# Kernel tuning notes

Hardware: AMD Instinct MI355X
Metric: run time of the kernel (lower is better)

Reference implementation:

```python
import jax, jax.numpy as jnp
import numpy as np

N_NODES = 100000
N_EDGES = 1600000
IN_DIM = 8
EMB = 50
NUM_TASK = 112
NUM_LAYER = 2
BN_EPS = 1e-5


def setup_inputs() -> dict:
    key = jax.random.key(0)
    ks = jax.random.split(key, 12)
    s = 0.1  # weight init scale
    L, D = NUM_LAYER, EMB
    return {
        "src": jax.random.randint(ks[0], (N_EDGES,), 0, N_NODES),
        "dst": jax.random.randint(ks[1], (N_EDGES,), 0, N_NODES),
        "node_feats": jax.random.normal(ks[2], (N_NODES, IN_DIM), jnp.float32),
        "edge_feats": jax.random.normal(ks[3], (N_EDGES, IN_DIM), jnp.float32),
        "node_W": jax.random.normal(ks[4], (IN_DIM, D), jnp.float32) * s,
        "node_b": jnp.zeros((D,), jnp.float32),
        "edge_W": jax.random.normal(ks[5], (IN_DIM, D), jnp.float32) * s,
        "edge_b": jnp.zeros((D,), jnp.float32),
        "eps": jnp.zeros((L,), jnp.float32),
        "W1": jax.random.normal(ks[6], (L, D, 2 * D), jnp.float32) * s,
        "b1": jnp.zeros((L, 2 * D), jnp.float32),
        "g1": jnp.ones((L, 2 * D), jnp.float32),
        "be1": jnp.zeros((L, 2 * D), jnp.float32),
        "W2": jax.random.normal(ks[7], (L, 2 * D, D), jnp.float32) * s,
        "b2": jnp.zeros((L, D), jnp.float32),
        "g2": jnp.ones((L, D), jnp.float32),
        "be2": jnp.zeros((L, D), jnp.float32),
        "pred_W": jax.random.normal(ks[8], (D, NUM_TASK), jnp.float32) * s,
        "pred_b": jnp.zeros((NUM_TASK,), jnp.float32),
    }


def _bn(x, gamma, beta):
    # BatchNorm1d in training mode: batch mean, biased variance, eps=1e-5
    mu = jnp.mean(x, axis=0)
    var = jnp.mean(jnp.square(x - mu), axis=0)
    return (x - mu) * jax.lax.rsqrt(var + BN_EPS) * gamma + beta


def reference(src, dst, node_feats, edge_feats, node_W, node_b, edge_W, edge_b,
              eps, W1, b1, g1, be1, W2, b2, g2, be2, pred_W, pred_b):
    N = node_feats.shape[0]
    h = node_feats @ node_W + node_b          # [N, D] node encoder
    e = edge_feats @ edge_W + edge_b          # [E, D] edge encoder
    deg = jax.ops.segment_sum(jnp.ones(src.shape, h.dtype), dst, num_segments=N)
    inv_deg = jnp.where(deg > 0, 1.0 / jnp.maximum(deg, 1.0), 0.0)[:, None]  # mean; 0 for isolated nodes
    for i in range(W1.shape[0]):
        m = h[src] + e                                          # u_add_e
        agg = jax.ops.segment_sum(m, dst, num_segments=N) * inv_deg  # mean reduce
        h = (1.0 + eps[i]) * h + agg                            # eps-combine
        h = jax.nn.relu(_bn(h @ W1[i] + b1[i], g1[i], be1[i]))
        h = jax.nn.relu(_bn(h @ W2[i] + b2[i], g2[i], be2[i]))
    return h @ pred_W + pred_b                # [N, num_task]
```

## Files before the change

### kernel.cpp

```cpp
#include <hip/hip_runtime.h>
#include <hip/hip_bf16.h>

#define N_NODES 100000
#define N_EDGES 1600000
#define IN_DIM 8
#define D 50
#define D2 100
#define NTASK 112
#define BN_EPS 1e-5f
#define NBLK ((N_NODES + 255) / 256)
#define HS 56
#define SLOT 48

#define PARTS 8
#define NPP (N_NODES / PARTS)
#define SF_BPP 128
typedef int i4 __attribute__((ext_vector_type(4)));
typedef __attribute__((ext_vector_type(8))) short s16x8;
typedef __attribute__((ext_vector_type(4))) float f32x4;

__device__ __forceinline__ unsigned bf16_rn(float x) {
    unsigned u = __float_as_uint(x);
    return (u + 0x7fffu + ((u >> 16) & 1u)) >> 16;
}
__device__ __forceinline__ unsigned pack_bf16(float a, float b) {
    return bf16_rn(a) | (bf16_rn(b) << 16);
}

__global__ __launch_bounds__(256) void node_enc_pair(
    const float* __restrict__ nf, const float* __restrict__ nW,
    const float* __restrict__ nb, float* __restrict__ h,
    unsigned* __restrict__ hb) {
    __shared__ float sW[IN_DIM * D];
    __shared__ float sb[D];
    __shared__ float snf[10 * IN_DIM];
    int t = threadIdx.x;
    int n0 = blockIdx.x * 10;
    for (int i = t; i < IN_DIM * D; i += 256) sW[i] = nW[i];
    for (int i = t; i < D; i += 256) sb[i] = nb[i];
    for (int i = t; i < 10 * IN_DIM; i += 256) {
        int g = n0 * IN_DIM + i;
        snf[i] = (g < N_NODES * IN_DIM) ? nf[g] : 0.0f;
    }
    __syncthreads();
    if (t >= 250) return;
    int n = t / 25, j2 = t % 25;
    int g = n0 + n;
    if (g >= N_NODES) return;
    int j0 = 2 * j2, j1 = j0 + 1;
    float v0 = sb[j0], v1 = sb[j1];
#pragma unroll
    for (int k = 0; k < IN_DIM; k++) {
        float f = snf[n * IN_DIM + k];
        v0 += f * sW[k * D + j0];
        v1 += f * sW[k * D + j1];
    }
    *(float2*)&h[(size_t)g * HS + j0] = make_float2(v0, v1);
    if (hb) hb[(size_t)g * 32 + j2] = pack_bf16(v0, v1);
}

__global__ __launch_bounds__(256) void k_slotfill_part(
    const int* __restrict__ src, const int* __restrict__ dst,
    int* __restrict__ degi, int2* __restrict__ slots) {
    const int part = blockIdx.x & (PARTS - 1);
    const int blk = blockIdx.x >> 3;
    const int lo = part * NPP, hi = lo + NPP;
    const int NT = SF_BPP * 256;
    const int NG = N_EDGES / 4;
    const i4* s4 = (const i4*)src;
    const i4* d4 = (const i4*)dst;
    for (int g = blk * 256 + (int)threadIdx.x; g < NG; g += NT) {
        i4 dd = __builtin_nontemporal_load(d4 + g);
        i4 ss = __builtin_nontemporal_load(s4 + g);
#pragma unroll
        for (int k = 0; k < 4; k++) {
            int d = dd[k];
            if (d >= lo && d < hi) {
                int pos = atomicAdd(&degi[d], 1);
                if (pos < SLOT) slots[(size_t)d * SLOT + pos] = make_int2(ss[k], 4 * g + k);
            }
        }
    }
}

__global__ __launch_bounds__(256) void k_aggef_slot(
    const int* __restrict__ degi, const int2* __restrict__ slots,
    const float* __restrict__ ef, float* __restrict__ aggef) {
    int lane = threadIdx.x & 63, wv = threadIdx.x >> 6;
    int n = (blockIdx.x & 7) * NPP + (blockIdx.x >> 3) * 4 + wv;
    if (n >= N_NODES) return;
    int deg = degi[n];
    if (deg > SLOT) deg = SLOT;
    int g = lane >> 3, k = lane & 7;
    float a = 0.0f;
    for (int q = g; q < deg; q += 8) {
        int e = slots[(size_t)n * SLOT + q].y;
        a += ef[(size_t)e * 8 + k];
    }
    a += __shfl_xor(a, 8, 64);
    a += __shfl_xor(a, 16, 64);
    a += __shfl_xor(a, 32, 64);
    if (lane < 8) aggef[(size_t)n * 8 + lane] = a;
}

template<bool USE_HB>
__global__ __launch_bounds__(256) void gather_slot(
    const int* __restrict__ degi, const int2* __restrict__ slots,
    const float* __restrict__ aggef, const float* __restrict__ eW,
    const float* __restrict__ eb, const float* __restrict__ h,
    const unsigned* __restrict__ hb, const float* __restrict__ epsArr,
    int layer, float* __restrict__ hnew) {
    __shared__ float sW[IN_DIM * D];
    __shared__ float sB[D];
    int t = threadIdx.x;
    for (int i = t; i < IN_DIM * D; i += 256) sW[i] = eW[i];
    for (int i = t; i < D; i += 256) sB[i] = eb[i];
    __syncthreads();
    int lane = t & 63, wv = t >> 6, half = lane >> 5, li = lane & 31;
    int part = blockIdx.x & 7, bi = blockIdx.x >> 3;
    int r = bi * 8 + wv * 2 + half;
    if (r >= NPP) return;
    int n = part * NPP + r;
    int deg = degi[n];
    if (deg > SLOT) deg = SLOT;
    float iv = (deg > 0) ? (1.0f / (float)deg) : 0.0f;
    const int2* srow = &slots[(size_t)n * SLOT];
    float ax0 = 0, ay0 = 0, ax1 = 0, ay1 = 0;
    int p = 0;
    if (USE_HB) {
        for (; p + 8 <= deg; p += 8) {
            int4 q0 = *(const int4*)&srow[p];
            int4 q1 = *(const int4*)&srow[p + 2];
            int4 q2 = *(const int4*)&srow[p + 4];
            int4 q3 = *(const int4*)&srow[p + 6];
            if (li < 25) {
                unsigned w;
                w = hb[(size_t)q0.x * 32 + li]; ax0 += __uint_as_float(w << 16); ay0 += __uint_as_float(w & 0xffff0000u);
                w = hb[(size_t)q0.z * 32 + li]; ax1 += __uint_as_float(w << 16); ay1 += __uint_as_float(w & 0xffff0000u);
                w = hb[(size_t)q1.x * 32 + li]; ax0 += __uint_as_float(w << 16); ay0 += __uint_as_float(w & 0xffff0000u);
                w = hb[(size_t)q1.z * 32 + li]; ax1 += __uint_as_float(w << 16); ay1 += __uint_as_float(w & 0xffff0000u);
                w = hb[(size_t)q2.x * 32 + li]; ax0 += __uint_as_float(w << 16); ay0 += __uint_as_float(w & 0xffff0000u);
                w = hb[(size_t)q2.z * 32 + li]; ax1 += __uint_as_float(w << 16); ay1 += __uint_as_float(w & 0xffff0000u);
                w = hb[(size_t)q3.x * 32 + li]; ax0 += __uint_as_float(w << 16); ay0 += __uint_as_float(w & 0xffff0000u);
                w = hb[(size_t)q3.z * 32 + li]; ax1 += __uint_as_float(w << 16); ay1 += __uint_as_float(w & 0xffff0000u);
            }
        }
        if (p < deg) {
            int4 q0 = *(const int4*)&srow[p];
            int4 q1 = *(const int4*)&srow[p + 2];
            int4 q2 = *(const int4*)&srow[p + 4];
            int4 q3 = *(const int4*)&srow[p + 6];
            if (li < 25) {
                unsigned w;
                w = hb[(size_t)q0.x * 32 + li]; ax0 += __uint_as_float(w << 16); ay0 += __uint_as_float(w & 0xffff0000u);
                if (p + 1 < deg) { w = hb[(size_t)q0.z * 32 + li]; ax1 += __uint_as_float(w << 16); ay1 += __uint_as_float(w & 0xffff0000u); }
                if (p + 2 < deg) { w = hb[(size_t)q1.x * 32 + li]; ax0 += __uint_as_float(w << 16); ay0 += __uint_as_float(w & 0xffff0000u); }
                if (p + 3 < deg) { w = hb[(size_t)q1.z * 32 + li]; ax1 += __uint_as_float(w << 16); ay1 += __uint_as_float(w & 0xffff0000u); }
                if (p + 4 < deg) { w = hb[(size_t)q2.x * 32 + li]; ax0 += __uint_as_float(w << 16); ay0 += __uint_as_float(w & 0xffff0000u); }
                if (p + 5 < deg) { w = hb[(size_t)q2.z * 32 + li]; ax1 += __uint_as_float(w << 16); ay1 += __uint_as_float(w & 0xffff0000u); }
                if (p + 6 < deg) { w = hb[(size_t)q3.x * 32 + li]; ax0 += __uint_as_float(w << 16); ay0 += __uint_as_float(w & 0xffff0000u); }
            }
        }
    } else {
        for (; p < deg; p += 4) {
            int4 q0 = *(const int4*)&srow[p];
            int4 q1 = *(const int4*)&srow[p + 2];
            if (li < 25) {
                float2 v = *(const float2*)&h[(size_t)q0.x * HS + 2 * li];
                ax0 += v.x; ay0 += v.y;
                if (p + 1 < deg) {
                    v = *(const float2*)&h[(size_t)q0.z * HS + 2 * li];
                    ax1 += v.x; ay1 += v.y;
                }
                if (p + 2 < deg) {
                    v = *(const float2*)&h[(size_t)q1.x * HS + 2 * li];
                    ax0 += v.x; ay0 += v.y;
                }
                if (p + 3 < deg) {
                    v = *(const float2*)&h[(size_t)q1.z * HS + 2 * li];
                    ax1 += v.x; ay1 += v.y;
                }
            }
        }
    }
    if (li < 25) {
        float accx = ax0 + ax1, accy = ay0 + ay1;
        int j0 = 2 * li, j1 = j0 + 1;
        float e0 = 0.0f, e1 = 0.0f;
        if (deg > 0) {
            const float* ag = &aggef[(size_t)n * 8];
            float s0 = 0.0f, s1 = 0.0f;
#pragma unroll
            for (int k = 0; k < 8; k++) {
                float a = ag[k];
                s0 += a * sW[k * D + j0];
                s1 += a * sW[k * D + j1];
            }
            e0 = s0 * iv + sB[j0];
            e1 = s1 * iv + sB[j1];
        }
        float epsv = 1.0f + epsArr[layer];
        float2 hv = *(const float2*)&h[(size_t)n * HS + j0];
        float2 o;
        o.x = epsv * hv.x + iv * accx + e0;
        o.y = epsv * hv.y + iv * accy + e1;
        *(float2*)&hnew[(size_t)n * D + j0] = o;
    }
}

template<int K, int KP, int J, int JP, bool BN_IN, bool STATS>
__global__ __launch_bounds__(256) void gemm_mfma(
    const float* __restrict__ X, const float* __restrict__ W,
    const float* __restrict__ bias,
    const float* __restrict__ bnS, const float* __restrict__ bnQ,
    const float* __restrict__ bnG, const float* __restrict__ bnB,
    float* __restrict__ Y, float* __restrict__ sg, float* __restrict__ qg,
    int ntiles) {
    constexpr int RB = 64;
    constexpr int WS = KP + 8;
    constexpr int KS = KP / 32;
    constexpr int NCT = JP / 16;
    constexpr int KH = K / 2;
    constexpr int JH = JP / 2;
    constexpr bool RAGGED = (N_NODES % RB) != 0;
    __shared__ __align__(16) unsigned short shA_hi[RB * WS];
    __shared__ __align__(16) unsigned short shA_lo[RB * WS];
    __shared__ __align__(16) unsigned short sWT_hi[JP * WS];
    __shared__ __align__(16) unsigned short sWT_lo[JP * WS];
    __shared__ float sb[JP];
    __shared__ float sa[BN_IN ? K : 1], sc[BN_IN ? K : 1];
    __shared__ float sp[JP], qp[JP];
    int t = threadIdx.x;
    for (int i = t; i < RB * WS; i += 256) { shA_hi[i] = 0; shA_lo[i] = 0; }
    for (int i = t; i < JP * WS; i += 256) { sWT_hi[i] = 0; sWT_lo[i] = 0; }
    __syncthreads();
    for (int i = t; i < KP * JH; i += 256) {
        int k = i / JH, jj = i % JH;
        int j = 2 * jj;
        float2 w2 = make_float2(0.0f, 0.0f);
        if (k < K) {
            if (j + 1 < J) w2 = *(const float2*)&W[k * J + j];
            else if (j < J) w2.x = W[k * J + j];
        }
        unsigned ux = __float_as_uint(w2.x), uy = __float_as_uint(w2.y);
        sWT_hi[j * WS + k]       = (unsigned short)(ux >> 16);
        sWT_hi[(j + 1) * WS + k] = (unsigned short)(uy >> 16);
        float rx = w2.x - __uint_as_float(ux & 0xffff0000u);
        float ry = w2.y - __uint_as_float(uy & 0xffff0000u);
        sWT_lo[j * WS + k]       = (unsigned short)bf16_rn(rx);
        sWT_lo[(j + 1) * WS + k] = (unsigned short)bf16_rn(ry);
    }
    for (int i = t; i < JP; i += 256) sb[i] = (i < J) ? bias[i] : 0.0f;
    if (BN_IN) {
        const float invN = 1.0f / (float)N_NODES;
        for (int i = t; i < K; i += 256) {
            float mu = bnS[i] * invN;
            float var = bnQ[i] * invN - mu * mu;
            float rs = rsqrtf(var + BN_EPS);
            float a = bnG[i] * rs;
            sa[i] = a;
            sc[i] = bnB[i] - mu * a;
        }
    }
    if (STATS) {
        for (int i = t; i < JP; i += 256) { sp[i] = 0.0f; qp[i] = 0.0f; }
    }
    int lane = t & 63, wv = t >> 6;
    int lrow = lane & 15, lkg = lane >> 4;
    float sacc[NCT], qacc[NCT];
#pragma unroll
    for (int c = 0; c < NCT; c++) { sacc[c] = 0.0f; qacc[c] = 0.0f; }
    for (int tile = blockIdx.x; tile < ntiles; tile += gridDim.x) {
        __syncthreads();
        int base = tile * RB;
        for (int i = t; i < RB * KH; i += 256) {
            int r = i / KH, m = i % KH;
            int k = 2 * m;
            float2 v2 = make_float2(0.0f, 0.0f);
            if (!RAGGED || base + r < N_NODES)
                v2 = *(const float2*)&X[(size_t)(base + r) * K + k];
            if (BN_IN) {
                v2.x = fmaxf(v2.x * sa[k] + sc[k], 0.0f);
                v2.y = fmaxf(v2.y * sa[k + 1] + sc[k + 1], 0.0f);
            }
            unsigned ux = __float_as_uint(v2.x), uy = __float_as_uint(v2.y);
            *(unsigned*)&shA_hi[r * WS + k] = (ux >> 16) | (uy & 0xffff0000u);
            float rx = v2.x - __uint_as_float(ux & 0xffff0000u);
            float ry = v2.y - __uint_as_float(uy & 0xffff0000u);
            *(unsigned*)&shA_lo[r * WS + k] = bf16_rn(rx) | (bf16_rn(ry) << 16);
        }
        __syncthreads();
        s16x8 ah[KS], al[KS];
        int arow = wv * 16 + lrow;
#pragma unroll
        for (int ks = 0; ks < KS; ks++) {
            int off = arow * WS + ks * 32 + lkg * 8;
            ah[ks] = *(const s16x8*)&shA_hi[off];
            al[ks] = *(const s16x8*)&shA_lo[off];
        }
#pragma unroll
        for (int ct = 0; ct < NCT; ct++) {
            f32x4 a0 = {0.f, 0.f, 0.f, 0.f};
            f32x4 a1 = {0.f, 0.f, 0.f, 0.f};
            f32x4 a2 = {0.f, 0.f, 0.f, 0.f};
#pragma unroll
            for (int ks = 0; ks < KS; ks++) {
                int boff = (ct * 16 + lrow) * WS + ks * 32 + lkg * 8;
                s16x8 bh = *(const s16x8*)&sWT_hi[boff];
                s16x8 bl = *(const s16x8*)&sWT_lo[boff];
                a0 = __builtin_amdgcn_mfma_f32_16x16x32_bf16(ah[ks], bh, a0, 0, 0, 0);
                a1 = __builtin_amdgcn_mfma_f32_16x16x32_bf16(ah[ks], bl, a1, 0, 0, 0);
                a2 = __builtin_amdgcn_mfma_f32_16x16x32_bf16(al[ks], bh, a2, 0, 0, 0);
            }
            int col = ct * 16 + lrow;
#pragma unroll
            for (int j = 0; j < 4; j++) {
                int gn = base + wv * 16 + lkg * 4 + j;
                if (!RAGGED || gn < N_NODES) {
                    float v = a0[j] + (a1[j] + a2[j]) + sb[col];
                    if (col < J) Y[(size_t)gn * J + col] = v;
                    if (STATS) { sacc[ct] += v; qacc[ct] += v * v; }
                }
            }
        }
    }
    if (STATS) {
        __syncthreads();
#pragma unroll
        for (int c = 0; c < NCT; c++) {
            atomicAdd(&sp[c * 16 + (t & 15)], sacc[c]);
            atomicAdd(&qp[c * 16 + (t & 15)], qacc[c]);
        }
        __syncthreads();
        for (int i = t; i < J; i += 256) {
            atomicAdd(&sg[i], sp[i]);
            atomicAdd(&qg[i], qp[i]);
        }
    }
}

__global__ __launch_bounds__(256) void apply2_pair(
    const float* __restrict__ y2, const float* __restrict__ sr,
    const float* __restrict__ qr, const float* __restrict__ g,
    const float* __restrict__ be, float* __restrict__ h,
    unsigned* __restrict__ hb) {
    __shared__ float sa[D], sc[D];
    int t = threadIdx.x;
    if (t < D) {
        float invN = 1.0f / (float)N_NODES;
        float mu = sr[t] * invN;
        float var = qr[t] * invN - mu * mu;
        float rs = rsqrtf(var + BN_EPS);
        float a = g[t] * rs;
        sa[t] = a;
        sc[t] = be[t] - mu * a;
    }
    __syncthreads();
    int idx = blockIdx.x * 256 + t;
    if (idx >= N_NODES * 25) return;
    int n = idx / 25, j2 = idx % 25;
    int j0 = 2 * j2, j1 = j0 + 1;
    float2 y = *(const float2*)&y2[(size_t)n * D + j0];
    float v0 = fmaxf(y.x * sa[j0] + sc[j0], 0.0f);
    float v1 = fmaxf(y.y * sa[j1] + sc[j1], 0.0f);
    *(float2*)&h[(size_t)n * HS + j0] = make_float2(v0, v1);
    if (hb) hb[(size_t)n * 32 + j2] = pack_bf16(v0, v1);
}

__global__ void k_deg(const int* __restrict__ dst, int* __restrict__ degi) {
    int e = blockIdx.x * blockDim.x + threadIdx.x;
    if (e < N_EDGES) atomicAdd(&degi[dst[e]], 1);
}
__global__ void k_bsum(const int* __restrict__ degi, int* __restrict__ bsum) {
    __shared__ int lds[256];
    int t = threadIdx.x, i = blockIdx.x * 256 + t;
    lds[t] = (i < N_NODES) ? degi[i] : 0;
    __syncthreads();
    for (int s = 128; s > 0; s >>= 1) {
        if (t < s) lds[t] += lds[t + s];
        __syncthreads();
    }
    if (t == 0) bsum[blockIdx.x] = lds[0];
}
__global__ void k_bscan(const int* __restrict__ bsum, int* __restrict__ bpre) {
    __shared__ int lds[512];
    int t = threadIdx.x;
    int x = (t < NBLK) ? bsum[t] : 0;
    lds[t] = x;
    __syncthreads();
    int acc = x;
    for (int s = 1; s < 512; s <<= 1) {
        int add = (t >= s) ? lds[t - s] : 0;
        __syncthreads();
        acc += add;
        lds[t] = acc;
        __syncthreads();
    }
    if (t < NBLK) bpre[t] = acc - x;
}
__global__ void k_off(int* __restrict__ degi, const int* __restrict__ bpre,
                      int* __restrict__ off, float* __restrict__ invd) {
    __shared__ int lds[256];
    int t = threadIdx.x, i = blockIdx.x * 256 + t;
    int dv = (i < N_NODES) ? degi[i] : 0;
    lds[t] = dv;
    __syncthreads();
    int acc = dv;
    for (int s = 1; s < 256; s <<= 1) {
        int add = (t >= s) ? lds[t - s] : 0;
        __syncthreads();
        acc += add;
        lds[t] = acc;
        __syncthreads();
    }
    int excl = acc - dv + bpre[blockIdx.x];
    if (i < N_NODES) {
        off[i] = excl;
        degi[i] = excl;
        invd[i] = (dv > 0) ? (1.0f / (float)dv) : 0.0f;
    }
    if (i == 0) off[N_NODES] = N_EDGES;
}
__global__ void k_fill(const int* __restrict__ src, const int* __restrict__ dst,
                       int* __restrict__ cursor, int2* __restrict__ adj) {
    int e = blockIdx.x * blockDim.x + threadIdx.x;
    if (e >= N_EDGES) return;
    int d = dst[e];
    int pos = atomicAdd(&cursor[d], 1);
    adj[pos] = make_int2(src[e], e);
}
__global__ __launch_bounds__(256) void k_aggef_csr(
    const int* __restrict__ off, const int2* __restrict__ adj,
    const float* __restrict__ ef, float* __restrict__ aggef) {
    int lane = threadIdx.x & 63, wv = threadIdx.x >> 6;
    int n = blockIdx.x * 4 + wv;
    if (n >= N_NODES) return;
    int p0 = off[n], pend = off[n + 1];
    int g = lane >> 3, k = lane & 7;
    float a = 0.0f;
    for (int q = p0 + g; q < pend; q += 8) a += ef[(size_t)adj[q].y * 8 + k];
    a += __shfl_xor(a, 8, 64);
    a += __shfl_xor(a, 16, 64);
    a += __shfl_xor(a, 32, 64);
    if (lane < 8) aggef[(size_t)n * 8 + lane] = a;
}
__global__ __launch_bounds__(256) void gather_csr(
    const int* __restrict__ off, const int2* __restrict__ adj,
    const float* __restrict__ aggef, const float* __restrict__ eW,
    const float* __restrict__ eb, const float* __restrict__ h,
    const float* __restrict__ invd, const float* __restrict__ epsArr,
    int layer, float* __restrict__ hnew) {
    __shared__ float sW[IN_DIM * D];
    __shared__ float sB[D];
    int t = threadIdx.x;
    for (int i = t; i < IN_DIM * D; i += 256) sW[i] = eW[i];
    for (int i = t; i < D; i += 256) sB[i] = eb[i];
    __syncthreads();
    int lane = t & 63, wv = t >> 6;
    int n = blockIdx.x * 4 + wv;
    if (n >= N_NODES) return;
    int dd = (lane < D) ? lane : (D - 1);
    int p = off[n], pend = off[n + 1];
    int deg = pend - p;
    float acc = 0.0f;
    while (p + 4 <= pend) {
        int s0 = adj[p].x, s1 = adj[p + 1].x, s2 = adj[p + 2].x, s3 = adj[p + 3].x;
        acc += h[(size_t)s0 * HS + dd] + h[(size_t)s1 * HS + dd]
             + h[(size_t)s2 * HS + dd] + h[(size_t)s3 * HS + dd];
        p += 4;
    }
    while (p < pend) { acc += h[(size_t)adj[p].x * HS + dd]; p++; }
    if (lane < D) {
        float iv = invd[n];
        float extra = 0.0f;
        if (deg > 0) {
            const float* ag = &aggef[(size_t)n * 8];
            float s = 0.0f;
#pragma unroll
            for (int k = 0; k < 8; k++) s += ag[k] * sW[k * D + dd];
            extra = s * iv + sB[dd];
        }
        float epsv = 1.0f + epsArr[layer];
        hnew[(size_t)n * D + lane] = epsv * h[(size_t)n * HS + lane] + iv * acc + extra;
    }
}

extern "C" void kernel_launch(void* const* d_in, const int* in_sizes, int n_in,
                              void* d_out, int out_size, void* d_ws, size_t ws_size,
                              hipStream_t stream) {
    const int*   src        = (const int*)d_in[0];
    const int*   dst        = (const int*)d_in[1];
    const float* node_feats = (const float*)d_in[2];
    const float* edge_feats = (const float*)d_in[3];
    const float* node_W     = (const float*)d_in[4];
    const float* node_b     = (const float*)d_in[5];
    const float* edge_W     = (const float*)d_in[6];
    const float* edge_b     = (const float*)d_in[7];
    const float* epsArr     = (const float*)d_in[8];
    const float* W1         = (const float*)d_in[9];
    const float* b1         = (const float*)d_in[10];
    const float* g1         = (const float*)d_in[11];
    const float* be1        = (const float*)d_in[12];
    const float* W2         = (const float*)d_in[13];
    const float* b2         = (const float*)d_in[14];
    const float* g2         = (const float*)d_in[15];
    const float* be2        = (const float*)d_in[16];
    const float* pred_W     = (const float*)d_in[17];
    const float* pred_b     = (const float*)d_in[18];
    float* out = (float*)d_out;

    float* ws = (float*)d_ws;
    unsigned* hb = nullptr;
    float *h, *tmp, *invd = nullptr, *st, *aggef;
    int *degi, *off = nullptr, *bsum = nullptr, *bpre = nullptr;
    int2 *slots = nullptr, *adj = nullptr;

    auto layout = [&](int mode) -> size_t {
        float* p = ws;
        hb = nullptr; slots = nullptr; adj = nullptr;
        off = nullptr; bsum = nullptr; bpre = nullptr; invd = nullptr;
        if (mode == 2) { hb = (unsigned*)p; p += (size_t)N_NODES * 32; }
        h = p;    p += (size_t)N_NODES * HS;
        tmp = p;  p += (size_t)N_NODES * D;
        st = p;   p += 768;
        if (mode == 0) { invd = p; p += N_NODES; }
        int* ip = (int*)p;
        degi = ip; ip += N_NODES;
        char* end;
        if (mode >= 1) {
            slots = (int2*)ip;
            aggef = (float*)(slots + (size_t)N_NODES * SLOT);
            end = (char*)(aggef + (size_t)N_NODES * 8);
        } else {
            off = ip;  ip += N_NODES + 1;
            bsum = ip; ip += NBLK;
            bpre = ip; ip += NBLK + 1;
            adj = (int2*)ip;
            aggef = (float*)(adj + N_EDGES);
            end = (char*)(aggef + (size_t)N_NODES * 8);
        }
        return (size_t)(end - (char*)d_ws);
    };
    int mode = 2;
    if (ws_size < layout(2)) { mode = 1; if (ws_size < layout(1)) { mode = 0; layout(0); } }

    float* s1 = st, *q1 = st + 128, *s2 = st + 256, *q2 = st + 320;
    float* y1 = out;

    node_enc_pair<<<10000, 256, 0, stream>>>(node_feats, node_W, node_b, h, hb);
    hipMemsetAsync(degi, 0, N_NODES * sizeof(int), stream);

    const int GATHER_GRID = PARTS * ((NPP + 7) / 8);
    if (mode >= 1) {
        k_slotfill_part<<<PARTS * SF_BPP, 256, 0, stream>>>(src, dst, degi, slots);
        k_aggef_slot<<<(N_NODES + 3) / 4, 256, 0, stream>>>(degi, slots, edge_feats, aggef);
    } else {
        k_deg<<<(N_EDGES + 255) / 256, 256, 0, stream>>>(dst, degi);
        k_bsum<<<NBLK, 256, 0, stream>>>(degi, bsum);
        k_bscan<<<1, 512, 0, stream>>>(bsum, bpre);
        k_off<<<NBLK, 256, 0, stream>>>(degi, bpre, off, invd);
        k_fill<<<(N_EDGES + 255) / 256, 256, 0, stream>>>(src, dst, degi, adj);
        k_aggef_csr<<<(N_NODES + 3) / 4, 256, 0, stream>>>(off, adj, edge_feats, aggef);
    }

    const int NT64 = (N_NODES + 63) / 64;
    for (int layer = 0; layer < 2; layer++) {
        hipMemsetAsync(st, 0, 384 * sizeof(float), stream);
        if (mode == 2)
            gather_slot<true><<<GATHER_GRID, 256, 0, stream>>>(
                degi, slots, aggef, edge_W, edge_b, h, hb, epsArr, layer, tmp);
        else if (mode == 1)
            gather_slot<false><<<GATHER_GRID, 256, 0, stream>>>(
                degi, slots, aggef, edge_W, edge_b, h, nullptr, epsArr, layer, tmp);
        else
            gather_csr<<<(N_NODES + 3) / 4, 256, 0, stream>>>(
                off, adj, aggef, edge_W, edge_b, h, invd, epsArr, layer, tmp);
        gemm_mfma<50, 64, 100, 112, false, true><<<768, 256, 0, stream>>>(
            tmp, W1 + layer * D * D2, b1 + layer * D2, st, st, st, st, y1, s1, q1, NT64);
        gemm_mfma<100, 128, 50, 64, true, true><<<512, 256, 0, stream>>>(
            y1, W2 + layer * D2 * D, b2 + layer * D,
            s1, q1, g1 + layer * D2, be1 + layer * D2, tmp, s2, q2, NT64);
        if (layer == 0)
            apply2_pair<<<(N_NODES * 25 + 255) / 256, 256, 0, stream>>>(
                tmp, s2, q2, g2, be2, h, hb);
    }
    gemm_mfma<50, 64, 112, 112, true, false><<<768, 256, 0, stream>>>(
        tmp, pred_W, pred_b, s2, q2, g2 + D, be2 + D, out, st, st, NT64);
}
```

Measured before the change: 593.8 us.

## Emit bf16 hi/lo split from gather and vectorize GEMM2 staging loads

```diff
diff --git a/kernel.cpp b/kernel.cpp
--- a/kernel.cpp
+++ b/kernel.cpp
@@ -109,7 +109,7 @@
     const float* __restrict__ aggef, const float* __restrict__ eW,
     const float* __restrict__ eb, const float* __restrict__ h,
     const unsigned* __restrict__ hb, const float* __restrict__ epsArr,
-    int layer, float* __restrict__ hnew) {
+    int layer, unsigned* __restrict__ out_hi, unsigned* __restrict__ out_lo) {
     __shared__ float sW[IN_DIM * D];
     __shared__ float sB[D];
     int t = threadIdx.x;
@@ -201,17 +201,21 @@
         }
         float epsv = 1.0f + epsArr[layer];
         float2 hv = *(const float2*)&h[(size_t)n * HS + j0];
-        float2 o;
-        o.x = epsv * hv.x + iv * accx + e0;
-        o.y = epsv * hv.y + iv * accy + e1;
-        *(float2*)&hnew[(size_t)n * D + j0] = o;
-    }
-}
-
-template<int K, int KP, int J, int JP, bool BN_IN, bool STATS>
+        float ox = epsv * hv.x + iv * accx + e0;
+        float oy = epsv * hv.y + iv * accy + e1;
+        unsigned ux = __float_as_uint(ox), uy = __float_as_uint(oy);
+        out_hi[(size_t)n * 25 + li] = (ux >> 16) | (uy & 0xffff0000u);
+        float rx = ox - __uint_as_float(ux & 0xffff0000u);
+        float ry = oy - __uint_as_float(uy & 0xffff0000u);
+        out_lo[(size_t)n * 25 + li] = bf16_rn(rx) | (bf16_rn(ry) << 16);
+    }
+}
+
+template<int K, int KP, int J, int JP, int STAGE, bool BN_IN, bool STATS>
 __global__ __launch_bounds__(256) void gemm_mfma(
-    const float* __restrict__ X, const float* __restrict__ W,
-    const float* __restrict__ bias,
+    const float* __restrict__ X, const unsigned* __restrict__ Xhi,
+    const unsigned* __restrict__ Xlo,
+    const float* __restrict__ W, const float* __restrict__ bias,
     const float* __restrict__ bnS, const float* __restrict__ bnQ,
     const float* __restrict__ bnG, const float* __restrict__ bnB,
     float* __restrict__ Y, float* __restrict__ sg, float* __restrict__ qg,
@@ -220,7 +224,6 @@
     constexpr int WS = KP + 8;
     constexpr int KS = KP / 32;
     constexpr int NCT = JP / 16;
-    constexpr int KH = K / 2;
     constexpr int JH = JP / 2;
     constexpr bool RAGGED = (N_NODES % RB) != 0;
     __shared__ __align__(16) unsigned short shA_hi[RB * WS];
@@ -273,21 +276,62 @@
     for (int tile = blockIdx.x; tile < ntiles; tile += gridDim.x) {
         __syncthreads();
         int base = tile * RB;
-        for (int i = t; i < RB * KH; i += 256) {
-            int r = i / KH, m = i % KH;
-            int k = 2 * m;
-            float2 v2 = make_float2(0.0f, 0.0f);
-            if (!RAGGED || base + r < N_NODES)
-                v2 = *(const float2*)&X[(size_t)(base + r) * K + k];
-            if (BN_IN) {
-                v2.x = fmaxf(v2.x * sa[k] + sc[k], 0.0f);
-                v2.y = fmaxf(v2.y * sa[k + 1] + sc[k + 1], 0.0f);
-            }
-            unsigned ux = __float_as_uint(v2.x), uy = __float_as_uint(v2.y);
-            *(unsigned*)&shA_hi[r * WS + k] = (ux >> 16) | (uy & 0xffff0000u);
-            float rx = v2.x - __uint_as_float(ux & 0xffff0000u);
-            float ry = v2.y - __uint_as_float(uy & 0xffff0000u);
-            *(unsigned*)&shA_lo[r * WS + k] = bf16_rn(rx) | (bf16_rn(ry) << 16);
+        if constexpr (STAGE == 2) {
+            constexpr int KH = K / 2;
+            for (int i = t; i < RB * KH; i += 256) {
+                int r = i / KH, m = i % KH, k = 2 * m;
+                unsigned vh = 0, vl = 0;
+                if (!RAGGED || base + r < N_NODES) {
+                    vh = Xhi[(size_t)(base + r) * KH + m];
+                    vl = Xlo[(size_t)(base + r) * KH + m];
+                }
+                *(unsigned*)&shA_hi[r * WS + k] = vh;
+                *(unsigned*)&shA_lo[r * WS + k] = vl;
+            }
+        } else if constexpr (STAGE == 1) {
+            constexpr int KQ = K / 4;
+            for (int i = t; i < RB * KQ; i += 256) {
+                int r = i / KQ, m = i % KQ, k = 4 * m;
+                float4 v4 = make_float4(0.0f, 0.0f, 0.0f, 0.0f);
+                if (!RAGGED || base + r < N_NODES)
+                    v4 = *(const float4*)&X[(size_t)(base + r) * K + k];
+                if (BN_IN) {
+                    v4.x = fmaxf(v4.x * sa[k]     + sc[k],     0.0f);
+                    v4.y = fmaxf(v4.y * sa[k + 1] + sc[k + 1], 0.0f);
+                    v4.z = fmaxf(v4.z * sa[k + 2] + sc[k + 2], 0.0f);
+                    v4.w = fmaxf(v4.w * sa[k + 3] + sc[k + 3], 0.0f);
+                }
+                unsigned ux = __float_as_uint(v4.x), uy = __float_as_uint(v4.y);
+                unsigned uz = __float_as_uint(v4.z), uw = __float_as_uint(v4.w);
+                uint2 hi2, lo2;
+                hi2.x = (ux >> 16) | (uy & 0xffff0000u);
+                hi2.y = (uz >> 16) | (uw & 0xffff0000u);
+                float rx = v4.x - __uint_as_float(ux & 0xffff0000u);
+                float ry = v4.y - __uint_as_float(uy & 0xffff0000u);
+                float rz = v4.z - __uint_as_float(uz & 0xffff0000u);
+                float rw = v4.w - __uint_as_float(uw & 0xffff0000u);
+                lo2.x = bf16_rn(rx) | (bf16_rn(ry) << 16);
+                lo2.y = bf16_rn(rz) | (bf16_rn(rw) << 16);
+                *(uint2*)&shA_hi[r * WS + k] = hi2;
+                *(uint2*)&shA_lo[r * WS + k] = lo2;
+            }
+        } else {
+            constexpr int KH = K / 2;
+            for (int i = t; i < RB * KH; i += 256) {
+                int r = i / KH, m = i % KH, k = 2 * m;
+                float2 v2 = make_float2(0.0f, 0.0f);
+                if (!RAGGED || base + r < N_NODES)
+                    v2 = *(const float2*)&X[(size_t)(base + r) * K + k];
+                if (BN_IN) {
+                    v2.x = fmaxf(v2.x * sa[k] + sc[k], 0.0f);
+                    v2.y = fmaxf(v2.y * sa[k + 1] + sc[k + 1], 0.0f);
+                }
+                unsigned ux = __float_as_uint(v2.x), uy = __float_as_uint(v2.y);
+                *(unsigned*)&shA_hi[r * WS + k] = (ux >> 16) | (uy & 0xffff0000u);
+                float rx = v2.x - __uint_as_float(ux & 0xffff0000u);
+                float ry = v2.y - __uint_as_float(uy & 0xffff0000u);
+                *(unsigned*)&shA_lo[r * WS + k] = bf16_rn(rx) | (bf16_rn(ry) << 16);
+            }
         }
         __syncthreads();
         s16x8 ah[KS], al[KS];
@@ -546,6 +590,8 @@
 
     float* s1 = st, *q1 = st + 128, *s2 = st + 256, *q2 = st + 320;
     float* y1 = out;
+    unsigned* tmp_hi = (unsigned*)tmp;
+    unsigned* tmp_lo = tmp_hi + (size_t)N_NODES * 25;
 
     node_enc_pair<<<10000, 256, 0, stream>>>(node_feats, node_W, node_b, h, hb);
     hipMemsetAsync(degi, 0, N_NODES * sizeof(int), stream);
@@ -568,22 +614,29 @@
         hipMemsetAsync(st, 0, 384 * sizeof(float), stream);
         if (mode == 2)
             gather_slot<true><<<GATHER_GRID, 256, 0, stream>>>(
-                degi, slots, aggef, edge_W, edge_b, h, hb, epsArr, layer, tmp);
+                degi, slots, aggef, edge_W, edge_b, h, hb, epsArr, layer, tmp_hi, tmp_lo);
         else if (mode == 1)
             gather_slot<false><<<GATHER_GRID, 256, 0, stream>>>(
-                degi, slots, aggef, edge_W, edge_b, h, nullptr, epsArr, layer, tmp);
+                degi, slots, aggef, edge_W, edge_b, h, nullptr, epsArr, layer, tmp_hi, tmp_lo);
         else
             gather_csr<<<(N_NODES + 3) / 4, 256, 0, stream>>>(
                 off, adj, aggef, edge_W, edge_b, h, invd, epsArr, layer, tmp);
-        gemm_mfma<50, 64, 100, 112, false, true><<<768, 256, 0, stream>>>(
-            tmp, W1 + layer * D * D2, b1 + layer * D2, st, st, st, st, y1, s1, q1, NT64);
-        gemm_mfma<100, 128, 50, 64, true, true><<<512, 256, 0, stream>>>(
-            y1, W2 + layer * D2 * D, b2 + layer * D,
+        if (mode >= 1)
+            gemm_mfma<50, 64, 100, 112, 2, false, true><<<768, 256, 0, stream>>>(
+                nullptr, tmp_hi, tmp_lo, W1 + layer * D * D2, b1 + layer * D2,
+                st, st, st, st, y1, s1, q1, NT64);
+        else
+            gemm_mfma<50, 64, 100, 112, 0, false, true><<<768, 256, 0, stream>>>(
+                tmp, nullptr, nullptr, W1 + layer * D * D2, b1 + layer * D2,
+                st, st, st, st, y1, s1, q1, NT64);
+        gemm_mfma<100, 128, 50, 64, 1, true, true><<<512, 256, 0, stream>>>(
+            y1, nullptr, nullptr, W2 + layer * D2 * D, b2 + layer * D,
             s1, q1, g1 + layer * D2, be1 + layer * D2, tmp, s2, q2, NT64);
         if (layer == 0)
             apply2_pair<<<(N_NODES * 25 + 255) / 256, 256, 0, stream>>>(
                 tmp, s2, q2, g2, be2, h, hb);
     }
-    gemm_mfma<50, 64, 112, 112, true, false><<<768, 256, 0, stream>>>(
-        tmp, pred_W, pred_b, s2, q2, g2 + D, be2 + D, out, st, st, NT64);
-}
+    gemm_mfma<50, 64, 112, 112, 0, true, false><<<768, 256, 0, stream>>>(
+        tmp, nullptr, nullptr, pred_W, pred_b, s2, q2, g2 + D, be2 + D,
+        out, st, st, NT64);
+}
```

New measurement: 580.4 us. 2.3% less time.
